# Performance work log

Hardware: AMD Instinct MI355X
Metric: run time of the kernel (lower is better)

## Reference

```python
import jax, jax.numpy as jnp
import numpy as np
import math, itertools

DIM = 384; KEY_DIM = 16; HEADS = 8; ATTN_RATIO = 4; RES = 28
RES2 = math.ceil(RES / 2)            # 14
NH_KD = KEY_DIM * HEADS              # 128
D = ATTN_RATIO * KEY_DIM             # 64
DH = D * HEADS                       # 512
N = RES * RES                        # 784
N2 = RES2 * RES2                     # 196
OUT_DIM = DIM
SCALE = KEY_DIM ** -0.5
BATCH = 64


def build_bias_idxs():
    stride = math.ceil(RES / RES2)
    offsets = {}
    idxs = []
    for p1 in itertools.product(range(RES2), repeat=2):
        for p2 in itertools.product(range(RES), repeat=2):
            off = (abs(p1[0] * stride - p2[0]), abs(p1[1] * stride - p2[1]))
            if off not in offsets:
                offsets[off] = len(offsets)
            idxs.append(offsets[off])
    return np.asarray(idxs, dtype=np.int32), len(offsets)


def dwconv(x, w, b, stride):
    # depthwise 3x3, padding 1; x: (B,C,H,W), w: (C,1,3,3)
    y = jax.lax.conv_general_dilated(
        x, w, (stride, stride), ((1, 1), (1, 1)),
        dimension_numbers=("NCHW", "OIHW", "NCHW"),
        feature_group_count=x.shape[1])
    return y + b[None, :, None, None]


def conv1x1(x, w, b):
    return jnp.einsum("bchw,oc->bohw", x, w) + b[None, :, None, None]


def bn(x, s, o):
    # inference-mode BatchNorm folded to per-channel scale/offset
    return x * s[None, :, None, None] + o[None, :, None, None]


def setup_inputs() -> dict:
    key = jax.random.key(0)
    ks = jax.random.split(key, 25)
    def rn(k, shape, sc=0.05):
        return jax.random.normal(k, shape, jnp.float32) * sc
    idxs, n_off = build_bias_idxs()
    return dict(
        x=jax.random.normal(ks[0], (BATCH, DIM, RES, RES), jnp.float32),
        ql_w=rn(ks[1], (DIM, 1, 3, 3)), ql_b=rn(ks[2], (DIM,)),
        qp_w=rn(ks[3], (NH_KD, DIM)), qp_b=rn(ks[4], (NH_KD,)),
        qp_s=1.0 + rn(ks[5], (NH_KD,)), qp_o=rn(ks[6], (NH_KD,)),
        k_w=rn(ks[7], (NH_KD, DIM)), k_b=rn(ks[8], (NH_KD,)),
        k_s=1.0 + rn(ks[9], (NH_KD,)), k_o=rn(ks[10], (NH_KD,)),
        v_w=rn(ks[11], (DH, DIM)), v_b=rn(ks[12], (DH,)),
        v_s=1.0 + rn(ks[13], (DH,)), v_o=rn(ks[14], (DH,)),
        vl_w=rn(ks[15], (DH, 1, 3, 3)), vl_b=rn(ks[16], (DH,)),
        vl_s=1.0 + rn(ks[17], (DH,)), vl_o=rn(ks[18], (DH,)),
        p_w=rn(ks[19], (OUT_DIM, DH)), p_b=rn(ks[20], (OUT_DIM,)),
        p_s=1.0 + rn(ks[21], (OUT_DIM,)), p_o=rn(ks[22], (OUT_DIM,)),
        ab=rn(ks[23], (HEADS, n_off)),
        bias_idxs=jnp.asarray(idxs),
    )


def reference(x, ql_w, ql_b, qp_w, qp_b, qp_s, qp_o,
              k_w, k_b, k_s, k_o, v_w, v_b, v_s, v_o,
              vl_w, vl_b, vl_s, vl_o, p_w, p_b, p_s, p_o,
              ab, bias_idxs):
    B = x.shape[0]
    # LGQuery: depthwise stride-2 conv + stride-2 avg-pool(k=1), then 1x1 conv + BN
    local_q = dwconv(x, ql_w, ql_b, 2)
    pool_q = x[:, :, ::2, ::2]               # AvgPool2d(1, 2, 0)
    q = bn(conv1x1(local_q + pool_q, qp_w, qp_b), qp_s, qp_o)
    q = q.reshape(B, HEADS, KEY_DIM, N2).transpose(0, 1, 3, 2)   # (B,H,N2,kd)

    k = bn(conv1x1(x, k_w, k_b), k_s, k_o).reshape(B, HEADS, KEY_DIM, N)  # (B,H,kd,N)

    v = bn(conv1x1(x, v_w, v_b), v_s, v_o)   # (B,DH,RES,RES)
    v_local = bn(dwconv(v, vl_w, vl_b, 2), vl_s, vl_o)           # (B,DH,RES2,RES2)
    v = v.reshape(B, HEADS, D, N).transpose(0, 1, 3, 2)          # (B,H,N,d)

    bias = ab[:, bias_idxs].reshape(HEADS, N2, N)                # gathered rel-pos bias
    attn = jnp.einsum("bhqc,bhck->bhqk", q, k) * SCALE + bias[None]
    attn = jax.nn.softmax(attn, axis=-1)

    out = jnp.einsum("bhqk,bhkd->bhqd", attn, v).transpose(0, 1, 3, 2)
    out = out.reshape(B, DH, RES2, RES2) + v_local
    out = bn(conv1x1(jax.nn.gelu(out, approximate=False), p_w, p_b), p_s, p_o)
    return out
```

## Files before the change

### kernel.cpp

```cpp
#include <hip/hip_runtime.h>
#include <math.h>

#define BATCH   64
#define DIMC    384
#define KEY_DIM 16
#define HEADS   8
#define DD      64
#define DH      512
#define NH_KD   128
#define RES     28
#define RES2    14
#define NN      784
#define NN2     196
#define OUT_DIM 384
#define SCALE   0.25f
#define LOG2E   1.44269504088896340736f
#define XPAD    896
#define QPAD    256
#define KPAD    832
#define XSP     796

typedef __attribute__((ext_vector_type(8))) short bf16x8;
typedef __attribute__((ext_vector_type(4))) float f32x4;

#define MFMA32(a, b, c) __builtin_amdgcn_mfma_f32_16x16x32_bf16(a, b, c, 0, 0, 0)
#define SWZ(row, bcol) ((row) * 64 + ((bcol) ^ ((((row) >> 1) & 3) << 4)))

__device__ inline short f2bf(float f) {
    unsigned u = __float_as_uint(f);
    unsigned r = (u + 0x7fff + ((u >> 16) & 1)) >> 16;
    return (short)r;
}
__device__ inline float bf2f(short h) {
    return __uint_as_float(((unsigned)(unsigned short)h) << 16);
}
__device__ __forceinline__ unsigned cvt_pk_bf16(float a, float b) {
    unsigned r;
    asm("v_cvt_pk_bf16_f32 %0, %1, %2" : "=v"(r) : "v"(a), "v"(b));
    return r;
}
__device__ __forceinline__ float fexp2(float x) {
    float r;
    asm("v_exp_f32 %0, %1" : "=v"(r) : "v"(x));
    return r;
}
__device__ __forceinline__ void gload16(const void* g, void* l) {
    __builtin_amdgcn_global_load_lds((const __attribute__((address_space(1))) void*)g,
                                     (__attribute__((address_space(3))) void*)l, 16, 0, 0);
}

#define O_XT_HI    0u
#define O_QINT_HI  44040192u
#define O_QT       88080384u
#define O_KT       96468992u
#define O_V        123731968u
#define O_VLT      178257920u
#define O_BIASB    203948032u
#define O_W_HI     206557184u
#define O_W_LO     207540224u
#define O_ATTNT    0u
#define O_GT_HI    25690112u

__global__ __launch_bounds__(256)
void xprep_kernel(const float* __restrict__ x, const float* __restrict__ ql_w,
                  const float* __restrict__ ql_b, short* __restrict__ xT,
                  short* __restrict__ qinT) {
    __shared__ short xs[32 * XSP];
    const int cg = blockIdx.x, b = blockIdx.y;
    const int t = threadIdx.x;
    const float* xb = x + ((size_t)b * DIMC + cg * 32) * NN;

    {
        const int c = t >> 3, sub = t & 7;
        const float* xc = xb + (size_t)c * NN;
        short* dst = xs + c * XSP;
        #pragma unroll 5
        for (int p4 = sub; p4 < 196; p4 += 8) {
            float4 v = *(const float4*)(xc + p4 * 4);
            uint2 pk = {cvt_pk_bf16(v.x, v.y), cvt_pk_bf16(v.z, v.w)};
            *(uint2*)(dst + p4 * 4) = pk;
        }
    }
    __syncthreads();

    {
        const int c_l = t & 31;
        const int ng  = t >> 5;
        const short* src = xs + c_l * XSP;
        short* dstb = xT + (size_t)b * XPAD * DIMC + cg * 32 + c_l;
        for (int n = ng; n < NN; n += 8)
            dstb[(size_t)n * DIMC] = src[n];
        for (int n = NN + ng; n < XPAD; n += 8)
            dstb[(size_t)n * DIMC] = 0;
    }

    {
        const int c_l = t & 31;
        const int ng  = t >> 5;
        const int c = cg * 32 + c_l;
        const short* xc = xs + c_l * XSP;
        const float* w = ql_w + c * 9;
        const float w0 = w[0], w1 = w[1], w2 = w[2], w3 = w[3], w4 = w[4],
                    w5 = w[5], w6 = w[6], w7 = w[7], w8 = w[8];
        const float bias = ql_b[c];
        short* qdst = qinT + (size_t)b * QPAD * DIMC + c;
        for (int n2 = ng; n2 < NN2; n2 += 8) {
            int i = n2 / RES2, j = n2 % RES2;
            int r0 = 2 * i - 1, c0 = 2 * j - 1;
            float acc = bias;
            if (r0 >= 0) {
                if (c0 >= 0)       acc += bf2f(xc[r0 * RES + c0])     * w0;
                                   acc += bf2f(xc[r0 * RES + c0 + 1]) * w1;
                if (c0 + 2 < RES)  acc += bf2f(xc[r0 * RES + c0 + 2]) * w2;
            }
            {
                if (c0 >= 0)       acc += bf2f(xc[(r0 + 1) * RES + c0])     * w3;
                                   acc += bf2f(xc[(r0 + 1) * RES + c0 + 1]) * w4;
                if (c0 + 2 < RES)  acc += bf2f(xc[(r0 + 1) * RES + c0 + 2]) * w5;
            }
            if (r0 + 2 < RES) {
                if (c0 >= 0)       acc += bf2f(xc[(r0 + 2) * RES + c0])     * w6;
                                   acc += bf2f(xc[(r0 + 2) * RES + c0 + 1]) * w7;
                if (c0 + 2 < RES)  acc += bf2f(xc[(r0 + 2) * RES + c0 + 2]) * w8;
            }
            acc += bf2f(xc[(2 * i) * RES + 2 * j]);
            qdst[(size_t)n2 * DIMC] = f2bf(acc);
        }
        for (int n2 = NN2 + ng; n2 < QPAD; n2 += 8)
            qdst[(size_t)n2 * DIMC] = 0;
    }
}

__global__ void wsplit_kernel(const float* __restrict__ w0, const float* __restrict__ w1,
                              const float* __restrict__ w2, const float* __restrict__ w3,
                              short* __restrict__ hi, short* __restrict__ lo) {
    int i = blockIdx.x * 256 + threadIdx.x;
    if (i >= 491520) return;
    const float* src; int j = i;
    if (j < 49152) src = w0;
    else if (j < 98304) { src = w1; j -= 49152; }
    else if (j < 294912) { src = w2; j -= 98304; }
    else { src = w3; j -= 294912; }
    float v = src[j];
    short h = f2bf(v);
    hi[i] = h;
    lo[i] = f2bf(v - bf2f(h));
}

template<bool WLO, bool SWAP>
__global__ __launch_bounds__(256)
void gemm_split_kernel(const short* __restrict__ wgt_hi, const short* __restrict__ wgt_lo,
                       const short* __restrict__ act,
                       const float* __restrict__ bias, const float* __restrict__ s,
                       const float* __restrict__ off,
                       float* __restrict__ out_f, short* __restrict__ out_b,
                       int mode, int C, int Nn, int Npad, int NPADo, float pscale,
                       int NXn, int NYo, int O) {
    constexpr int NT = 2 + (WLO ? 1 : 0);
    constexpr int STRIDE = NT * 8192;
    constexpr int OFF_A = 0, OFF_B = 8192, OFF_WL = 16384;
    __shared__ __align__(1024) char LDS[2 * STRIDE];

    const int bid = blockIdx.x;
    const int xcd = bid & 7;
    const int g   = bid >> 3;
    const int ot  = g % NYo;
    const int pp  = (g / NYo) * 8 + xcd;
    const int nt  = pp % NXn;
    const int b   = pp / NXn;
    const int n0 = nt * 128, o0 = ot * 128;

    const int t = threadIdx.x;
    const int lane = t & 63, wid = t >> 6;
    const int wm = wid & 1, wn = wid >> 1;
    const int lr = lane & 15, kg = lane >> 4;

    const short* Ahi = SWAP ? act : wgt_hi;
    const short* Bhi = SWAP ? wgt_hi : act;

    f32x4 acc[4][4];
    #pragma unroll
    for (int m = 0; m < 4; ++m)
        #pragma unroll
        for (int n = 0; n < 4; ++n)
            acc[m][n] = (f32x4){0.f, 0.f, 0.f, 0.f};

    const int ccol = (lane & 3) * 16;
    const int r0   = wid * 32 + (lane >> 2);

    auto STAGE = [&](int buf, int k0) {
        char* base = LDS + buf * STRIDE;
        #pragma unroll
        for (int c = 0; c < 2; ++c) {
            int r = r0 + c * 16;
            int bcs = ccol ^ (((r >> 1) & 3) << 4);
            size_t aRow = SWAP ? ((size_t)b * Npad + n0 + r) : (size_t)(o0 + r);
            size_t bRow = SWAP ? (size_t)(o0 + r) : ((size_t)b * Npad + n0 + r);
            char* ldsc = base + wid * 2048 + c * 1024;
            gload16((const char*)Ahi + (aRow * C + k0) * 2 + bcs, ldsc + OFF_A);
            gload16((const char*)Bhi + (bRow * C + k0) * 2 + bcs, ldsc + OFF_B);
            if constexpr (WLO)
                gload16((const char*)wgt_lo + ((size_t)(o0 + r) * C + k0) * 2 + bcs, ldsc + OFF_WL);
        }
    };

    STAGE(0, 0);
    int cur = 0;
    __syncthreads();

    for (int k0 = 0;; k0 += 32) {
        const bool hasNext = (k0 + 32 < C);
        if (hasNext) STAGE(cur ^ 1, k0 + 32);

        char* cb = LDS + cur * STRIDE;
        bf16x8 ah[4], wlm[4];
        #pragma unroll
        for (int m = 0; m < 4; ++m) {
            int row = wm * 64 + m * 16 + lr;
            ah[m] = *(const bf16x8*)(cb + OFF_A + SWZ(row, kg * 16));
            if constexpr (WLO) if (!SWAP) wlm[m] = *(const bf16x8*)(cb + OFF_WL + SWZ(row, kg * 16));
        }
        #pragma unroll
        for (int nf = 0; nf < 4; ++nf) {
            int row = wn * 64 + nf * 16 + lr;
            bf16x8 bh = *(const bf16x8*)(cb + OFF_B + SWZ(row, kg * 16));
            bf16x8 blw;
            if constexpr (WLO) if (SWAP) blw = *(const bf16x8*)(cb + OFF_WL + SWZ(row, kg * 16));
            #pragma unroll
            for (int m = 0; m < 4; ++m) {
                acc[m][nf] = MFMA32(ah[m], bh, acc[m][nf]);
                if constexpr (WLO) {
                    if (SWAP) acc[m][nf] = MFMA32(ah[m], blw, acc[m][nf]);
                    else      acc[m][nf] = MFMA32(wlm[m], bh, acc[m][nf]);
                }
            }
        }
        if (!hasNext) break;
        __syncthreads();
        cur ^= 1;
    }

    if (mode == 2) {
        #pragma unroll
        for (int m = 0; m < 4; ++m) {
            #pragma unroll
            for (int nf = 0; nf < 4; ++nf) {
                int col = n0 + wn * 64 + nf * 16 + lr;
                if (col >= NPADo) continue;
                int hh = (o0 + wm * 64 + m * 16) >> 4;
                bool nok = (col < Nn);
                float v[4];
                #pragma unroll
                for (int r = 0; r < 4; ++r) {
                    int row = o0 + wm * 64 + m * 16 + kg * 4 + r;
                    float a = s[row];
                    v[r] = nok ? (acc[m][nf][r] * a + (bias[row] * a + off[row])) * pscale : 0.f;
                }
                unsigned h01 = cvt_pk_bf16(v[0], v[1]);
                unsigned h23 = cvt_pk_bf16(v[2], v[3]);
                float l0 = v[0] - __uint_as_float(h01 << 16);
                float l1 = v[1] - __uint_as_float(h01 & 0xffff0000u);
                float l2 = v[2] - __uint_as_float(h23 << 16);
                float l3 = v[3] - __uint_as_float(h23 & 0xffff0000u);
                uint2 hst = {h01, h23};
                uint2 lst = {cvt_pk_bf16(l0, l1), cvt_pk_bf16(l2, l3)};
                size_t base = ((size_t)(b * 8 + hh) * NPADo + col) * 32 + kg * 4;
                *(uint2*)(out_b + base)      = hst;
                *(uint2*)(out_b + base + 16) = lst;
            }
        }
    } else {
        #pragma unroll
        for (int nf = 0; nf < 4; ++nf) {
            int col_d = o0 + wn * 64 + nf * 16 + lr;
            float a = s[col_d];
            float badd = bias[col_d] * a + off[col_d];
            #pragma unroll
            for (int m = 0; m < 4; ++m) {
                int rown = n0 + wm * 64 + m * 16 + kg * 4;
                float v0 = acc[m][nf][0] * a + badd;
                float v1 = acc[m][nf][1] * a + badd;
                float v2 = acc[m][nf][2] * a + badd;
                float v3 = acc[m][nf][3] * a + badd;
                if (mode == 0) {
                    if (rown < Nn) {
                        float4 vv = {v0, v1, v2, v3};
                        *(float4*)(out_f + ((size_t)b * O + col_d) * Nn + rown) = vv;
                    }
                } else {
                    if (rown + 3 < NPADo) {
                        uint2 st = {cvt_pk_bf16(v0, v1), cvt_pk_bf16(v2, v3)};
                        *(uint2*)(out_b + ((size_t)b * O + col_d) * NPADo + rown) = st;
                    }
                }
            }
        }
    }
}

__global__ __launch_bounds__(256)
void vlocalT_kernel(const short* __restrict__ v,
                    const float* __restrict__ vl_w, const float* __restrict__ vl_b,
                    const float* __restrict__ vl_s, const float* __restrict__ vl_o,
                    float* __restrict__ vlT) {
    __shared__ float tile[32][201];
    const int cg = blockIdx.x, b = blockIdx.y;
    const int t = threadIdx.x;
    {
        const int c_l = t >> 3, nsub = t & 7;
        const int c = cg * 32 + c_l;
        const size_t base = ((size_t)b * DH + c) * KPAD;
        const float* w = vl_w + c * 9;
        const float w0 = w[0], w1 = w[1], w2 = w[2], w3 = w[3], w4 = w[4],
                    w5 = w[5], w6 = w[6], w7 = w[7], w8 = w[8];
        const float bias = vl_b[c], sc = vl_s[c], of = vl_o[c];
        for (int n2 = nsub; n2 < NN2; n2 += 8) {
            int i = n2 / RES2, j = n2 % RES2;
            int r0 = 2 * i - 1, c0 = 2 * j - 1;
            float acc = bias;
            if (r0 >= 0) {
                if (c0 >= 0)       acc += bf2f(v[base + r0 * RES + c0])     * w0;
                                   acc += bf2f(v[base + r0 * RES + c0 + 1]) * w1;
                if (c0 + 2 < RES)  acc += bf2f(v[base + r0 * RES + c0 + 2]) * w2;
            }
            {
                if (c0 >= 0)       acc += bf2f(v[base + (r0 + 1) * RES + c0])     * w3;
                                   acc += bf2f(v[base + (r0 + 1) * RES + c0 + 1]) * w4;
                if (c0 + 2 < RES)  acc += bf2f(v[base + (r0 + 1) * RES + c0 + 2]) * w5;
            }
            if (r0 + 2 < RES) {
                if (c0 >= 0)       acc += bf2f(v[base + (r0 + 2) * RES + c0])     * w6;
                                   acc += bf2f(v[base + (r0 + 2) * RES + c0 + 1]) * w7;
                if (c0 + 2 < RES)  acc += bf2f(v[base + (r0 + 2) * RES + c0 + 2]) * w8;
            }
            tile[c_l][n2] = acc * sc + of;
        }
    }
    __syncthreads();
    {
        const int c_l = t & 31, ng = t >> 5;
        for (int n2 = ng; n2 < NN2; n2 += 8)
            vlT[((size_t)b * NN2 + n2) * DH + cg * 32 + c_l] = tile[c_l][n2];
    }
}

__global__ void biasB_expand_kernel(const float* __restrict__ ab, const int* __restrict__ bidx,
                                    short* __restrict__ biasB, int n_off) {
    int i = blockIdx.x * 256 + threadIdx.x;
    int h = blockIdx.y;
    if (i >= NN2 * KPAD) return;
    int q = i / KPAD, key = i - q * KPAD;
    short v = 0;
    if (key < NN) v = f2bf(ab[h * n_off + bidx[q * NN + key]] * LOG2E);
    biasB[(size_t)h * NN2 * KPAD + i] = v;
}

__global__ __launch_bounds__(512, 4)
void attn_mfma12_kernel(const short* __restrict__ QT, const short* __restrict__ KT,
                        const short* __restrict__ V, const short* __restrict__ biasB,
                        float* __restrict__ outT) {
    __shared__ __align__(1024) char LDS[2 * 12288 + 8 * 4096];

    const int t = threadIdx.x;
    const int bid = blockIdx.x;
    const int h = bid & 7;
    const int b = bid >> 3;

    const int lane = t & 63, wid = t >> 6;
    const int lr = lane & 15, kg = lane >> 4;
    const int wq0 = wid * 32;

    bf16x8 qb1[2], qb2[2];
    const short* bb[2];
    #pragma unroll
    for (int qf = 0; qf < 2; ++qf) {
        int qg = wq0 + qf * 16 + lr;
        const short* qrow = QT + ((size_t)(b * 8 + h) * QPAD + qg) * 32;
        qb1[qf] = *(const bf16x8*)(qrow + (kg & 1) * 8);
        qb2[qf] = (bf16x8){0, 0, 0, 0, 0, 0, 0, 0};
        if (kg < 2) qb2[qf] = *(const bf16x8*)(qrow + 16 + kg * 8);
        int qs = (qg < NN2) ? qg : (NN2 - 1);
        bb[qf] = biasB + ((size_t)h * NN2 + qs) * KPAD;
    }

    const short* kbase = KT + (size_t)(b * 8 + h) * KPAD * 32;
    const short* vbase = V + ((size_t)b * DH + h * DD) * KPAD;

    f32x4 acc[2][4];
    #pragma unroll
    for (int qf = 0; qf < 2; ++qf)
        #pragma unroll
        for (int nt = 0; nt < 4; ++nt)
            acc[qf][nt] = (f32x4){0.f, 0.f, 0.f, 0.f};
    float sacc[2] = {0.f, 0.f};
    char* PsW = LDS + 24576 + wid * 4096;
    const int swz = (lr & 7) << 4;

    auto STAGE = [&](int buf, int tile) {
        const int k0 = tile * 64;
        char* base = LDS + buf * 12288;
        #pragma unroll
        for (int ci = 0; ci < 2; ++ci) {
            if (ci == 1 && wid >= 4) continue;
            int chunk = (ci == 0) ? wid : wid + 8;
            if (chunk < 4) {
                int row = chunk * 16 + (lane >> 2);
                int pcol = (lane & 3) ^ ((row >> 1) & 3);
                gload16((const char*)(kbase + (size_t)(k0 + row) * 32) + pcol * 16,
                        base + chunk * 1024);
            } else {
                int vrow = (chunk - 4) * 8 + (lane >> 3);
                int pcol = (lane & 7) ^ (vrow & 7);
                gload16((const char*)(vbase + (size_t)vrow * KPAD + k0) + pcol * 16,
                        base + 4096 + (chunk - 4) * 1024);
            }
        }
    };

    auto COMPUTE = [&](int buf, int tile) {
        const int k0 = tile * 64;
        char* cb = LDS + buf * 12288;
        short4 b4[2][4];
        #pragma unroll
        for (int qf = 0; qf < 2; ++qf)
            #pragma unroll
            for (int nt = 0; nt < 4; ++nt)
                b4[qf][nt] = *(const short4*)(bb[qf] + k0 + nt * 16 + kg * 4);

        #pragma unroll
        for (int qf = 0; qf < 2; ++qf) {
            f32x4 sc[4];
            __builtin_amdgcn_s_setprio(1);
            #pragma unroll
            for (int nt = 0; nt < 4; ++nt) {
                int row = nt * 16 + lr;
                bf16x8 ka = *(const bf16x8*)(cb + row * 64 + ((kg ^ ((row >> 1) & 3)) * 16));
                sc[nt] = (f32x4){0.f, 0.f, 0.f, 0.f};
                sc[nt] = MFMA32(ka, qb1[qf], sc[nt]);
                sc[nt] = MFMA32(ka, qb2[qf], sc[nt]);
            }
            __builtin_amdgcn_s_setprio(0);

            char* Psw = PsW + qf * 2048;
            #pragma unroll
            for (int nt = 0; nt < 4; ++nt) {
                int keyb = k0 + nt * 16 + kg * 4;
                bool kvalid = keyb < NN;
                float pv[4];
                #pragma unroll
                for (int r = 0; r < 4; ++r) {
                    float sv = sc[nt][r] + bf2f(((const short*)&b4[qf][nt])[r]);
                    pv[r] = kvalid ? fexp2(sv) : 0.f;
                    sacc[qf] += pv[r];
                }
                uint2 pk2 = {cvt_pk_bf16(pv[0], pv[1]), cvt_pk_bf16(pv[2], pv[3])};
                *(uint2*)(Psw + lr * 128 + ((nt * 32 + kg * 8) ^ swz)) = pk2;
            }
        }

        #pragma unroll
        for (int ks = 0; ks < 2; ++ks) {
            bf16x8 vf[4];
            #pragma unroll
            for (int nt = 0; nt < 4; ++nt) {
                int row = nt * 16 + lr;
                int pk_ = ks * 4 + kg;
                vf[nt] = *(const bf16x8*)(cb + 4096 + row * 128 + ((pk_ ^ (row & 7)) * 16));
            }
            #pragma unroll
            for (int qf = 0; qf < 2; ++qf) {
                bf16x8 pa = *(const bf16x8*)(PsW + qf * 2048 + lr * 128
                                             + ((ks * 64 + kg * 16) ^ swz));
                __builtin_amdgcn_s_setprio(1);
                #pragma unroll
                for (int nt = 0; nt < 4; ++nt)
                    acc[qf][nt] = MFMA32(pa, vf[nt], acc[qf][nt]);
                __builtin_amdgcn_s_setprio(0);
            }
        }
    };

    STAGE(0, 0);
    int cur = 0;
    __syncthreads();
    #pragma unroll 1
    for (int tile = 0; tile < 13; ++tile) {
        if (tile + 1 < 13) STAGE(cur ^ 1, tile + 1);
        COMPUTE(cur, tile);
        __syncthreads();
        cur ^= 1;
    }

    #pragma unroll
    for (int qf = 0; qf < 2; ++qf) {
        float sv = sacc[qf];
        sv += __shfl_xor(sv, 16, 64);
        sv += __shfl_xor(sv, 32, 64);
        #pragma unroll
        for (int r = 0; r < 4; ++r) {
            int qrow_ = wq0 + qf * 16 + kg * 4 + r;
            if (qrow_ >= NN2) continue;
            float inv = 1.f / __shfl(sv, kg * 4 + r, 64);
            #pragma unroll
            for (int nt = 0; nt < 4; ++nt) {
                int d = nt * 16 + lr;
                outT[((size_t)b * NN2 + qrow_) * DH + h * DD + d] = acc[qf][nt][r] * inv;
            }
        }
    }
}

__global__ __launch_bounds__(256)
void geluE_kernel(const float* __restrict__ aT, const float* __restrict__ vlT,
                  short* __restrict__ gT) {
    int i = blockIdx.x * 256 + threadIdx.x;
    int d0 = (i & 63) * 8;
    int n2 = (i >> 6) & (QPAD - 1);
    int b  = i >> 14;
    short* gp = gT + ((size_t)b * QPAD + n2) * DH + d0;
    if (n2 >= NN2) {
        *(uint4*)gp = (uint4){0u, 0u, 0u, 0u};
        return;
    }
    size_t ao = ((size_t)b * NN2 + n2) * DH + d0;
    float4 a0 = *(const float4*)(aT + ao);
    float4 a1 = *(const float4*)(aT + ao + 4);
    float4 v0 = *(const float4*)(vlT + ao);
    float4 v1 = *(const float4*)(vlT + ao + 4);
    float s[8] = {a0.x + v0.x, a0.y + v0.y, a0.z + v0.z, a0.w + v0.w,
                  a1.x + v1.x, a1.y + v1.y, a1.z + v1.z, a1.w + v1.w};
    float g[8];
    #pragma unroll
    for (int k = 0; k < 8; ++k)
        g[k] = 0.5f * s[k] * (1.f + erff(s[k] * 0.70710678118654752440f));
    uint4 st = {cvt_pk_bf16(g[0], g[1]), cvt_pk_bf16(g[2], g[3]),
                cvt_pk_bf16(g[4], g[5]), cvt_pk_bf16(g[6], g[7])};
    *(uint4*)gp = st;
}

extern "C" void kernel_launch(void* const* d_in, const int* in_sizes, int n_in,
                              void* d_out, int out_size, void* d_ws, size_t ws_size,
                              hipStream_t stream) {
    const float* x     = (const float*)d_in[0];
    const float* ql_w  = (const float*)d_in[1];
    const float* ql_b  = (const float*)d_in[2];
    const float* qp_w  = (const float*)d_in[3];
    const float* qp_b  = (const float*)d_in[4];
    const float* qp_s  = (const float*)d_in[5];
    const float* qp_o  = (const float*)d_in[6];
    const float* k_w   = (const float*)d_in[7];
    const float* k_b   = (const float*)d_in[8];
    const float* k_s   = (const float*)d_in[9];
    const float* k_o   = (const float*)d_in[10];
    const float* v_w   = (const float*)d_in[11];
    const float* v_b   = (const float*)d_in[12];
    const float* v_s   = (const float*)d_in[13];
    const float* v_o   = (const float*)d_in[14];
    const float* vl_w  = (const float*)d_in[15];
    const float* vl_b  = (const float*)d_in[16];
    const float* vl_s  = (const float*)d_in[17];
    const float* vl_o  = (const float*)d_in[18];
    const float* p_w   = (const float*)d_in[19];
    const float* p_b   = (const float*)d_in[20];
    const float* p_s   = (const float*)d_in[21];
    const float* p_o   = (const float*)d_in[22];
    const float* ab    = (const float*)d_in[23];
    const int*   bidx  = (const int*)d_in[24];
    float* out = (float*)d_out;
    int n_off = in_sizes[23] / HEADS;

    char* ws = (char*)d_ws;
    short* qinT_h = (short*)(ws + O_QINT_HI);
    short* xT_h   = (short*)(ws + O_XT_HI);
    short* QT     = (short*)(ws + O_QT);
    short* KT     = (short*)(ws + O_KT);
    short* Vb     = (short*)(ws + O_V);
    float* vlT    = (float*)(ws + O_VLT);
    short* biasB  = (short*)(ws + O_BIASB);
    short* w_h    = (short*)(ws + O_W_HI);
    short* w_l    = (short*)(ws + O_W_LO);
    float* attnT  = (float*)(ws + O_ATTNT);
    short* gT_h   = (short*)(ws + O_GT_HI);

    xprep_kernel<<<dim3(DIMC / 32, BATCH), 256, 0, stream>>>(x, ql_w, ql_b, xT_h, qinT_h);
    wsplit_kernel<<<dim3(1920), 256, 0, stream>>>(qp_w, k_w, v_w, p_w, w_h, w_l);
    gemm_split_kernel<false, false><<<dim3(128), 256, 0, stream>>>(
        w_h + 0, nullptr, qinT_h, qp_b, qp_s, qp_o,
        nullptr, QT, 2, DIMC, NN2, QPAD, QPAD, SCALE * LOG2E, 2, 1, 128);
    gemm_split_kernel<false, false><<<dim3(448), 256, 0, stream>>>(
        w_h + 49152, nullptr, xT_h, k_b, k_s, k_o,
        nullptr, KT, 2, DIMC, NN, XPAD, KPAD, 1.0f, 7, 1, 128);
    gemm_split_kernel<false, true><<<dim3(1792), 256, 0, stream>>>(
        w_h + 98304, nullptr, xT_h, v_b, v_s, v_o,
        nullptr, Vb, 1, DIMC, NN, XPAD, KPAD, 1.0f, 7, 4, 512);
    vlocalT_kernel<<<dim3(DH / 32, BATCH), 256, 0, stream>>>(Vb, vl_w, vl_b, vl_s, vl_o, vlT);
    biasB_expand_kernel<<<dim3((NN2 * KPAD + 255) / 256, HEADS), 256, 0, stream>>>(ab, bidx, biasB, n_off);
    attn_mfma12_kernel<<<dim3(HEADS * BATCH), 512, 0, stream>>>(QT, KT, Vb, biasB, attnT);
    geluE_kernel<<<dim3(4096), 256, 0, stream>>>(attnT, vlT, gT_h);
    gemm_split_kernel<false, true><<<dim3(384), 256, 0, stream>>>(
        w_h + 294912, nullptr, gT_h, p_b, p_s, p_o,
        out, nullptr, 0, DH, NN2, QPAD, 0, 1.0f, 2, 3, 384);
}
```

Baseline: 262.6 us.

## Restructure attention kernel for higher occupancy and bf16 output

The attention kernel now processes each query fragment's P·V right after its softmax, so the per-wave P scratch shrinks to one 2 KB buffer and the launch-bound occupancy hint doubles. Padded keys get a -inf bias so the per-key validity check is removed, and the V fragments are reloaded per use instead of held in registers. The attention output is written as bf16 rather than fp32, which halves that intermediate's write and its read in the GELU kernel. This trades some extra LDS reads and a little precision in the attention output for lower register and LDS pressure and less memory traffic.

```diff
diff --git a/kernel.cpp b/kernel.cpp
--- a/kernel.cpp
+++ b/kernel.cpp
@@ -350,16 +350,16 @@
     int h = blockIdx.y;
     if (i >= NN2 * KPAD) return;
     int q = i / KPAD, key = i - q * KPAD;
-    short v = 0;
+    short v = (short)0xFF80;
     if (key < NN) v = f2bf(ab[h * n_off + bidx[q * NN + key]] * LOG2E);
     biasB[(size_t)h * NN2 * KPAD + i] = v;
 }
 
-__global__ __launch_bounds__(512, 4)
-void attn_mfma12_kernel(const short* __restrict__ QT, const short* __restrict__ KT,
+__global__ __launch_bounds__(512, 8)
+void attn_mfma13_kernel(const short* __restrict__ QT, const short* __restrict__ KT,
                         const short* __restrict__ V, const short* __restrict__ biasB,
-                        float* __restrict__ outT) {
-    __shared__ __align__(1024) char LDS[2 * 12288 + 8 * 4096];
+                        short* __restrict__ outT) {
+    __shared__ __align__(1024) char LDS[2 * 12288 + 8 * 2048];
 
     const int t = threadIdx.x;
     const int bid = blockIdx.x;
@@ -393,7 +393,7 @@
         for (int nt = 0; nt < 4; ++nt)
             acc[qf][nt] = (f32x4){0.f, 0.f, 0.f, 0.f};
     float sacc[2] = {0.f, 0.f};
-    char* PsW = LDS + 24576 + wid * 4096;
+    char* PsW = LDS + 24576 + wid * 2048;
     const int swz = (lr & 7) << 4;
 
     auto STAGE = [&](int buf, int tile) {
@@ -420,15 +420,14 @@
     auto COMPUTE = [&](int buf, int tile) {
         const int k0 = tile * 64;
         char* cb = LDS + buf * 12288;
-        short4 b4[2][4];
-        #pragma unroll
-        for (int qf = 0; qf < 2; ++qf)
+
+        #pragma unroll
+        for (int qf = 0; qf < 2; ++qf) {
+            short4 b4[4];
             #pragma unroll
             for (int nt = 0; nt < 4; ++nt)
-                b4[qf][nt] = *(const short4*)(bb[qf] + k0 + nt * 16 + kg * 4);
-
-        #pragma unroll
-        for (int qf = 0; qf < 2; ++qf) {
+                b4[nt] = *(const short4*)(bb[qf] + k0 + nt * 16 + kg * 4);
+
             f32x4 sc[4];
             __builtin_amdgcn_s_setprio(1);
             #pragma unroll
@@ -441,40 +440,30 @@
             }
             __builtin_amdgcn_s_setprio(0);
 
-            char* Psw = PsW + qf * 2048;
             #pragma unroll
             for (int nt = 0; nt < 4; ++nt) {
-                int keyb = k0 + nt * 16 + kg * 4;
-                bool kvalid = keyb < NN;
                 float pv[4];
                 #pragma unroll
                 for (int r = 0; r < 4; ++r) {
-                    float sv = sc[nt][r] + bf2f(((const short*)&b4[qf][nt])[r]);
-                    pv[r] = kvalid ? fexp2(sv) : 0.f;
+                    float sv = sc[nt][r] + bf2f(((const short*)&b4[nt])[r]);
+                    pv[r] = fexp2(sv);
                     sacc[qf] += pv[r];
                 }
                 uint2 pk2 = {cvt_pk_bf16(pv[0], pv[1]), cvt_pk_bf16(pv[2], pv[3])};
-                *(uint2*)(Psw + lr * 128 + ((nt * 32 + kg * 8) ^ swz)) = pk2;
-            }
-        }
-
-        #pragma unroll
-        for (int ks = 0; ks < 2; ++ks) {
-            bf16x8 vf[4];
-            #pragma unroll
-            for (int nt = 0; nt < 4; ++nt) {
-                int row = nt * 16 + lr;
-                int pk_ = ks * 4 + kg;
-                vf[nt] = *(const bf16x8*)(cb + 4096 + row * 128 + ((pk_ ^ (row & 7)) * 16));
-            }
-            #pragma unroll
-            for (int qf = 0; qf < 2; ++qf) {
-                bf16x8 pa = *(const bf16x8*)(PsW + qf * 2048 + lr * 128
-                                             + ((ks * 64 + kg * 16) ^ swz));
+                *(uint2*)(PsW + lr * 128 + ((nt * 32 + kg * 8) ^ swz)) = pk2;
+            }
+
+            #pragma unroll
+            for (int ks = 0; ks < 2; ++ks) {
+                bf16x8 pa = *(const bf16x8*)(PsW + lr * 128 + ((ks * 64 + kg * 16) ^ swz));
                 __builtin_amdgcn_s_setprio(1);
                 #pragma unroll
-                for (int nt = 0; nt < 4; ++nt)
-                    acc[qf][nt] = MFMA32(pa, vf[nt], acc[qf][nt]);
+                for (int nt = 0; nt < 4; ++nt) {
+                    int row = nt * 16 + lr;
+                    int pk_ = ks * 4 + kg;
+                    bf16x8 vf = *(const bf16x8*)(cb + 4096 + row * 128 + ((pk_ ^ (row & 7)) * 16));
+                    acc[qf][nt] = MFMA32(pa, vf, acc[qf][nt]);
+                }
                 __builtin_amdgcn_s_setprio(0);
             }
         }
@@ -501,17 +490,18 @@
             int qrow_ = wq0 + qf * 16 + kg * 4 + r;
             if (qrow_ >= NN2) continue;
             float inv = 1.f / __shfl(sv, kg * 4 + r, 64);
+            short* grow = outT + ((size_t)b * NN2 + qrow_) * DH + h * DD;
             #pragma unroll
             for (int nt = 0; nt < 4; ++nt) {
                 int d = nt * 16 + lr;
-                outT[((size_t)b * NN2 + qrow_) * DH + h * DD + d] = acc[qf][nt][r] * inv;
+                grow[d] = f2bf(acc[qf][nt][r] * inv);
             }
         }
     }
 }
 
 __global__ __launch_bounds__(256)
-void geluE_kernel(const float* __restrict__ aT, const float* __restrict__ vlT,
+void geluE_kernel(const short* __restrict__ aT, const float* __restrict__ vlT,
                   short* __restrict__ gT) {
     int i = blockIdx.x * 256 + threadIdx.x;
     int d0 = (i & 63) * 8;
@@ -523,12 +513,14 @@
         return;
     }
     size_t ao = ((size_t)b * NN2 + n2) * DH + d0;
-    float4 a0 = *(const float4*)(aT + ao);
-    float4 a1 = *(const float4*)(aT + ao + 4);
+    bf16x8 av = *(const bf16x8*)(aT + ao);
     float4 v0 = *(const float4*)(vlT + ao);
     float4 v1 = *(const float4*)(vlT + ao + 4);
-    float s[8] = {a0.x + v0.x, a0.y + v0.y, a0.z + v0.z, a0.w + v0.w,
-                  a1.x + v1.x, a1.y + v1.y, a1.z + v1.z, a1.w + v1.w};
+    float s[8];
+    #pragma unroll
+    for (int k = 0; k < 4; ++k) s[k] = bf2f(av[k]) + ((const float*)&v0)[k];
+    #pragma unroll
+    for (int k = 0; k < 4; ++k) s[4 + k] = bf2f(av[4 + k]) + ((const float*)&v1)[k];
     float g[8];
     #pragma unroll
     for (int k = 0; k < 8; ++k)
@@ -579,7 +571,7 @@
     short* biasB  = (short*)(ws + O_BIASB);
     short* w_h    = (short*)(ws + O_W_HI);
     short* w_l    = (short*)(ws + O_W_LO);
-    float* attnT  = (float*)(ws + O_ATTNT);
+    short* attnT  = (short*)(ws + O_ATTNT);
     short* gT_h   = (short*)(ws + O_GT_HI);
 
     xprep_kernel<<<dim3(DIMC / 32, BATCH), 256, 0, stream>>>(x, ql_w, ql_b, xT_h, qinT_h);
@@ -595,7 +587,7 @@
         nullptr, Vb, 1, DIMC, NN, XPAD, KPAD, 1.0f, 7, 4, 512);
     vlocalT_kernel<<<dim3(DH / 32, BATCH), 256, 0, stream>>>(Vb, vl_w, vl_b, vl_s, vl_o, vlT);
     biasB_expand_kernel<<<dim3((NN2 * KPAD + 255) / 256, HEADS), 256, 0, stream>>>(ab, bidx, biasB, n_off);
-    attn_mfma12_kernel<<<dim3(HEADS * BATCH), 512, 0, stream>>>(QT, KT, Vb, biasB, attnT);
+    attn_mfma13_kernel<<<dim3(HEADS * BATCH), 512, 0, stream>>>(QT, KT, Vb, biasB, attnT);
     geluE_kernel<<<dim3(4096), 256, 0, stream>>>(attnT, vlT, gT_h);
     gemm_split_kernel<false, true><<<dim3(384), 256, 0, stream>>>(
         w_h + 294912, nullptr, gT_h, p_b, p_s, p_o,
```

Measured after the change: 476.5 us. +81.5%, slower.
